# Performance work log

Measured on AMD Instinct MI355X. Metric: run time of the kernel, lower is better.

The kernel has to match this reference:

```python
import jax, jax.numpy as jnp
import numpy as np

B, DIM = 32768, 768
M, K = 128, 32          # num_subvectors, code_size
D = DIM // M            # subvector_dim = 6


def setup_inputs() -> dict:
    key = jax.random.key(0)
    kx, kc = jax.random.split(key)
    x = jax.random.normal(kx, (B, DIM), dtype=jnp.float32)
    codebooks = jax.random.normal(kc, (M, K, D), dtype=jnp.float32) * 0.01
    return {"x": x, "codebooks": codebooks}


def reference(x, codebooks):
    b = x.shape[0]
    m, k, d = codebooks.shape
    sub = x.reshape(b, m, d)                                   # (B, M, D)
    # per-subvector dot products with each code: (B, M, K)
    dots = jnp.einsum('bmd,mkd->bmk', sub, codebooks)
    soft = jax.nn.softmax(dots, axis=2)                        # (B, M, K)
    soft_q = jnp.einsum('bmk,mkd->bmd', soft, codebooks)       # (B, M, D)
    idx = jnp.argmax(dots, axis=2)                             # (B, M) int
    discrete = codebooks[jnp.arange(m)[None, :], idx]          # (B, M, D)
    # straight-through: forward = discrete, gradient flows through soft_q
    quant = soft_q - jax.lax.stop_gradient(soft_q - discrete)
    return quant.reshape(b, m * d)
```

## Files before the change

### kernel.cpp

```cpp
#include <hip/hip_runtime.h>


#define BATCH 32768
#define DIM   768
#define K_CB  32
#define D_SUB 6
#define KPT   8
#define BROWS 32
#define RSTG  8
#define HALFF 384
#define STGF  (RSTG*HALFF)

#define DPP_XOR1 0xB1
#define DPP_XOR2 0x4E

template<int CTRL>
__device__ __forceinline__ float dppf(float v) {
    return __int_as_float(__builtin_amdgcn_update_dpp(
        0, __float_as_int(v), CTRL, 0xF, 0xF, true));
}
template<int CTRL>
__device__ __forceinline__ int dppi(int v) {
    return __builtin_amdgcn_update_dpp(0, v, CTRL, 0xF, 0xF, true);
}

__global__ __launch_bounds__(256)
void pq_head_kernel(const float* __restrict__ x,
                    const float* __restrict__ cb,
                    float* __restrict__ out) {
    __shared__ float xs[STGF];

    const int t     = threadIdx.x;
    const int kq    = t & 3;
    const int mloc  = t >> 2;
    const int mhalf = blockIdx.y;
    const int m     = mhalf * 64 + mloc;
    const int b0    = blockIdx.x * BROWS;

    float c[KPT * D_SUB];
    {
        const float4* cb4 = reinterpret_cast<const float4*>(
            cb + ((size_t)m * K_CB + (size_t)kq * KPT) * D_SUB);
        #pragma unroll
        for (int i = 0; i < 12; ++i) {
            float4 v = cb4[i];
            c[4*i+0]=v.x; c[4*i+1]=v.y; c[4*i+2]=v.z; c[4*i+3]=v.w;
        }
    }

    const float* xh = x   + (size_t)mhalf * HALFF;
    float*       oh = out + (size_t)mhalf * HALFF;

    float4 pf[3];
    #pragma unroll
    for (int i = 0; i < 3; ++i) {
        int f   = (i * 256 + t) * 4;
        int r   = f / HALFF;
        int col = f - r * HALFF;
        pf[i] = *reinterpret_cast<const float4*>(xh + (size_t)(b0 + r) * DIM + col);
    }

    const int NSTG = BROWS / RSTG;
    for (int s = 0; s < NSTG; ++s) {
        __syncthreads();
        #pragma unroll
        for (int i = 0; i < 3; ++i)
            *reinterpret_cast<float4*>(&xs[(i * 256 + t) * 4]) = pf[i];
        __syncthreads();

        if (s + 1 < NSTG) {
            int rb = b0 + (s + 1) * RSTG;
            #pragma unroll
            for (int i = 0; i < 3; ++i) {
                int f   = (i * 256 + t) * 4;
                int r   = f / HALFF;
                int col = f - r * HALFF;
                pf[i] = *reinterpret_cast<const float4*>(xh + (size_t)(rb + r) * DIM + col);
            }
        }

        #pragma unroll
        for (int r = 0; r < RSTG; ++r) {
            const int b = b0 + s * RSTG + r;
            const float* xr = &xs[r * HALFF + mloc * D_SUB];
            float2 x01 = *reinterpret_cast<const float2*>(xr);
            float2 x23 = *reinterpret_cast<const float2*>(xr + 2);
            float2 x45 = *reinterpret_cast<const float2*>(xr + 4);
            float xv[6] = {x01.x, x01.y, x23.x, x23.y, x45.x, x45.y};

            float best1 = -3.402823466e+38f;
            float best2 = -3.402823466e+38f;
            int   kg    = kq * KPT;
            #pragma unroll
            for (int j = 0; j < KPT; ++j) {
                float d = c[j*6+0] * xv[0];
                #pragma unroll
                for (int e = 1; e < 6; ++e) d = fmaf(c[j*6+e], xv[e], d);
                bool gt = d > best1;
                best2 = gt ? best1 : fmaxf(best2, d);
                kg    = gt ? (kq * KPT + j) : kg;
                best1 = gt ? d : best1;
            }

            {
                float o1 = dppf<DPP_XOR1>(best1);
                float o2 = dppf<DPP_XOR1>(best2);
                int   ok = dppi<DPP_XOR1>(kg);
                bool take = (o1 > best1) || (o1 == best1 && ok < kg);
                best2 = fmaxf(fminf(best1, o1), fmaxf(best2, o2));
                kg    = take ? ok : kg;
                best1 = fmaxf(best1, o1);
            }
            {
                float o1 = dppf<DPP_XOR2>(best1);
                float o2 = dppf<DPP_XOR2>(best2);
                int   ok = dppi<DPP_XOR2>(kg);
                bool take = (o1 > best1) || (o1 == best1 && ok < kg);
                best2 = fmaxf(fminf(best1, o1), fmaxf(best2, o2));
                kg    = take ? ok : kg;
                best1 = fmaxf(best1, o1);
            }

            if (best1 - best2 < 1e-5f) {
                const float* crow = cb + (size_t)m * K_CB * D_SUB;
                double db = -1e300; int dkg = 0;
                for (int k2 = 0; k2 < K_CB; ++k2) {
                    double sa = 0.0;
                    for (int e = 0; e < 6; ++e)
                        sa = fma((double)crow[k2*6+e], (double)xv[e], sa);
                    if (sa > db) { db = sa; dkg = k2; }
                }
                kg = dkg;
            }

            const int j  = kg & 7;
            const bool s0 = (j & 1), s1b = (j & 2), s2b = (j & 4);
            float t1[4][D_SUB], t2[2][D_SUB], w[D_SUB];
            #pragma unroll
            for (int p = 0; p < 4; ++p)
                #pragma unroll
                for (int e = 0; e < 6; ++e)
                    t1[p][e] = s0 ? c[(2*p+1)*6+e] : c[(2*p)*6+e];
            #pragma unroll
            for (int p = 0; p < 2; ++p)
                #pragma unroll
                for (int e = 0; e < 6; ++e)
                    t2[p][e] = s1b ? t1[2*p+1][e] : t1[2*p][e];
            #pragma unroll
            for (int e = 0; e < 6; ++e)
                w[e] = s2b ? t2[1][e] : t2[0][e];

            if ((kg >> 3) == kq) {
                float* dst = oh + (size_t)b * DIM + mloc * D_SUB;
                float2* d2 = reinterpret_cast<float2*>(dst);
                d2[0] = make_float2(w[0], w[1]);
                d2[1] = make_float2(w[2], w[3]);
                d2[2] = make_float2(w[4], w[5]);
            }
        }
    }
}

extern "C" void kernel_launch(void* const* d_in, const int* in_sizes, int n_in,
                              void* d_out, int out_size, void* d_ws, size_t ws_size,
                              hipStream_t stream) {
    const float* x  = (const float*)d_in[0];
    const float* cb = (const float*)d_in[1];
    float* out = (float*)d_out;

    dim3 grid(BATCH / BROWS, 2);
    dim3 block(256);
    hipLaunchKernelGGL(pq_head_kernel, grid, block, 0, stream, x, cb, out);
}
```

Before: 258.1 us.

## Pack dot products into v2f FMAs, double-buffer LDS, gather outputs from global codebook

Packs pairs of codebook entries into 2-wide float vectors so two dot products are computed per packed FMA. It double-buffers the shared-memory staging to drop one barrier per stage, and halves rows per block while adding an occupancy hint to launch bounds. The select-tree of register muxes is replaced by a gather from the global codebook (cached) after all rows of a stage are resolved. Three of four lanes then each write one float2 of the output, so stores are coalesced across the quad. This adds dependent global loads per row and doubles the number of blocks.

```diff
diff --git a/kernel.cpp b/kernel.cpp
--- a/kernel.cpp
+++ b/kernel.cpp
@@ -1,13 +1,16 @@
 #include <hip/hip_runtime.h>
+#include <float.h>
 
+
+typedef float v2f __attribute__((ext_vector_type(2)));
 
 #define BATCH 32768
 #define DIM   768
 #define K_CB  32
 #define D_SUB 6
-#define KPT   8
-#define BROWS 32
+#define BROWS 16
 #define RSTG  8
+#define NSTG  (BROWS/RSTG)
 #define HALFF 384
 #define STGF  (RSTG*HALFF)
 
@@ -24,11 +27,11 @@
     return __builtin_amdgcn_update_dpp(0, v, CTRL, 0xF, 0xF, true);
 }
 
-__global__ __launch_bounds__(256)
+__global__ __launch_bounds__(256, 4)
 void pq_head_kernel(const float* __restrict__ x,
                     const float* __restrict__ cb,
                     float* __restrict__ out) {
-    __shared__ float xs[STGF];
+    __shared__ float xs[2][STGF];
 
     const int t     = threadIdx.x;
     const int kq    = t & 3;
@@ -37,69 +40,82 @@
     const int m     = mhalf * 64 + mloc;
     const int b0    = blockIdx.x * BROWS;
 
-    float c[KPT * D_SUB];
+    v2f cpk[4][D_SUB];
     {
+        float cc[48];
         const float4* cb4 = reinterpret_cast<const float4*>(
-            cb + ((size_t)m * K_CB + (size_t)kq * KPT) * D_SUB);
+            cb + ((size_t)m * K_CB + (size_t)kq * 8) * D_SUB);
         #pragma unroll
         for (int i = 0; i < 12; ++i) {
             float4 v = cb4[i];
-            c[4*i+0]=v.x; c[4*i+1]=v.y; c[4*i+2]=v.z; c[4*i+3]=v.w;
+            cc[4*i+0]=v.x; cc[4*i+1]=v.y; cc[4*i+2]=v.z; cc[4*i+3]=v.w;
         }
+        #pragma unroll
+        for (int p = 0; p < 4; ++p)
+            #pragma unroll
+            for (int e = 0; e < D_SUB; ++e)
+                cpk[p][e] = (v2f){cc[(2*p)*D_SUB + e], cc[(2*p+1)*D_SUB + e]};
     }
 
     const float* xh = x   + (size_t)mhalf * HALFF;
     float*       oh = out + (size_t)mhalf * HALFF;
 
+    int pr[3], pc[3];
+    #pragma unroll
+    for (int i = 0; i < 3; ++i) {
+        int f = (i * 256 + t) * 4;
+        pr[i] = f / HALFF;
+        pc[i] = f - pr[i] * HALFF;
+    }
+
     float4 pf[3];
     #pragma unroll
-    for (int i = 0; i < 3; ++i) {
-        int f   = (i * 256 + t) * 4;
-        int r   = f / HALFF;
-        int col = f - r * HALFF;
-        pf[i] = *reinterpret_cast<const float4*>(xh + (size_t)(b0 + r) * DIM + col);
-    }
+    for (int i = 0; i < 3; ++i)
+        pf[i] = *reinterpret_cast<const float4*>(xh + (size_t)(b0 + pr[i]) * DIM + pc[i]);
 
-    const int NSTG = BROWS / RSTG;
     for (int s = 0; s < NSTG; ++s) {
-        __syncthreads();
+        float* buf = xs[s & 1];
         #pragma unroll
         for (int i = 0; i < 3; ++i)
-            *reinterpret_cast<float4*>(&xs[(i * 256 + t) * 4]) = pf[i];
+            *reinterpret_cast<float4*>(&buf[(i * 256 + t) * 4]) = pf[i];
         __syncthreads();
 
         if (s + 1 < NSTG) {
             int rb = b0 + (s + 1) * RSTG;
             #pragma unroll
-            for (int i = 0; i < 3; ++i) {
-                int f   = (i * 256 + t) * 4;
-                int r   = f / HALFF;
-                int col = f - r * HALFF;
-                pf[i] = *reinterpret_cast<const float4*>(xh + (size_t)(rb + r) * DIM + col);
-            }
+            for (int i = 0; i < 3; ++i)
+                pf[i] = *reinterpret_cast<const float4*>(
+                    xh + (size_t)(rb + pr[i]) * DIM + pc[i]);
         }
 
+        int kg8[RSTG];
         #pragma unroll
         for (int r = 0; r < RSTG; ++r) {
-            const int b = b0 + s * RSTG + r;
-            const float* xr = &xs[r * HALFF + mloc * D_SUB];
+            const float* xr = &buf[r * HALFF + mloc * D_SUB];
             float2 x01 = *reinterpret_cast<const float2*>(xr);
             float2 x23 = *reinterpret_cast<const float2*>(xr + 2);
             float2 x45 = *reinterpret_cast<const float2*>(xr + 4);
             float xv[6] = {x01.x, x01.y, x23.x, x23.y, x45.x, x45.y};
+            v2f xxe[6];
+            #pragma unroll
+            for (int e = 0; e < 6; ++e) xxe[e] = (v2f){xv[e], xv[e]};
 
-            float best1 = -3.402823466e+38f;
-            float best2 = -3.402823466e+38f;
-            int   kg    = kq * KPT;
+            float best1 = -FLT_MAX, best2 = -FLT_MAX;
+            int   kg    = kq * 8;
             #pragma unroll
-            for (int j = 0; j < KPT; ++j) {
-                float d = c[j*6+0] * xv[0];
+            for (int p = 0; p < 4; ++p) {
+                v2f acc = cpk[p][0] * xxe[0];
                 #pragma unroll
-                for (int e = 1; e < 6; ++e) d = fmaf(c[j*6+e], xv[e], d);
-                bool gt = d > best1;
-                best2 = gt ? best1 : fmaxf(best2, d);
-                kg    = gt ? (kq * KPT + j) : kg;
-                best1 = gt ? d : best1;
+                for (int e = 1; e < 6; ++e)
+                    acc = __builtin_elementwise_fma(cpk[p][e], xxe[e], acc);
+                #pragma unroll
+                for (int h = 0; h < 2; ++h) {
+                    float d  = h ? acc.y : acc.x;
+                    bool  gt = d > best1;
+                    best2 = gt ? best1 : fmaxf(best2, d);
+                    kg    = gt ? (kq * 8 + 2*p + h) : kg;
+                    best1 = gt ? d : best1;
+                }
             }
 
             {
@@ -132,30 +148,25 @@
                 }
                 kg = dkg;
             }
+            kg8[r] = kg;
+        }
 
-            const int j  = kg & 7;
-            const bool s0 = (j & 1), s1b = (j & 2), s2b = (j & 4);
-            float t1[4][D_SUB], t2[2][D_SUB], w[D_SUB];
+        const bool act = (kq < 3);
+        float2 gv[RSTG];
+        if (act) {
             #pragma unroll
-            for (int p = 0; p < 4; ++p)
-                #pragma unroll
-                for (int e = 0; e < 6; ++e)
-                    t1[p][e] = s0 ? c[(2*p+1)*6+e] : c[(2*p)*6+e];
+            for (int r = 0; r < RSTG; ++r)
+                gv[r] = *(reinterpret_cast<const float2*>(
+                    cb + ((size_t)m * K_CB + (size_t)kg8[r]) * D_SUB) + kq);
+        }
+
+        __builtin_amdgcn_sched_barrier(0);
+
+        if (act) {
             #pragma unroll
-            for (int p = 0; p < 2; ++p)
-                #pragma unroll
-                for (int e = 0; e < 6; ++e)
-                    t2[p][e] = s1b ? t1[2*p+1][e] : t1[2*p][e];
-            #pragma unroll
-            for (int e = 0; e < 6; ++e)
-                w[e] = s2b ? t2[1][e] : t2[0][e];
-
-            if ((kg >> 3) == kq) {
-                float* dst = oh + (size_t)b * DIM + mloc * D_SUB;
-                float2* d2 = reinterpret_cast<float2*>(dst);
-                d2[0] = make_float2(w[0], w[1]);
-                d2[1] = make_float2(w[2], w[3]);
-                d2[2] = make_float2(w[4], w[5]);
+            for (int r = 0; r < RSTG; ++r) {
+                float* dst = oh + (size_t)(b0 + s * RSTG + r) * DIM + mloc * D_SUB;
+                *(reinterpret_cast<float2*>(dst) + kq) = gv[r];
             }
         }
     }
```

Measured after the change: 223.4 us. 1.16x faster.
